# Optimization experiments

Measured on AMD Instinct MI355X. Metric: run time of the kernel, lower is better.

## Reference

```python
import jax, jax.numpy as jnp
import numpy as np
from jax import lax

R, K = 1000, 80                 # proposals per image, foreground classes
IMG_H, IMG_W = 800.0, 1333.0    # image_shape (h, w) used by Boxes.clip
SCORE_THRESH = 0.05
NMS_THRESH = 0.5
TOPK = 100                      # topk_per_image


def setup_inputs() -> dict:
    key = jax.random.key(0)
    k1, k2, k3 = jax.random.split(key, 3)
    # well-formed class-specific boxes: x1y1 + positive wh
    x1y1 = jax.random.uniform(k1, (R, K, 2)) * jnp.array([IMG_W - 60.0, IMG_H - 60.0])
    wh = jax.random.uniform(k2, (R, K, 2)) * 200.0 + 10.0
    boxes = jnp.concatenate([x1y1, x1y1 + wh], axis=-1).reshape(R, K * 4)
    logits = jax.random.normal(k3, (R, K + 1)) * 2.0
    scores = jax.nn.softmax(logits, axis=-1)  # (R, K+1), last col = background
    return {"boxes": boxes, "scores": scores}


def _iou_matrix(b):
    # b: [R, 4] (x1, y1, x2, y2) -> [R, R] pairwise IoU
    x1, y1, x2, y2 = b[:, 0], b[:, 1], b[:, 2], b[:, 3]
    area = jnp.clip(x2 - x1, 0.0) * jnp.clip(y2 - y1, 0.0)
    xx1 = jnp.maximum(x1[:, None], x1[None, :])
    yy1 = jnp.maximum(y1[:, None], y1[None, :])
    xx2 = jnp.minimum(x2[:, None], x2[None, :])
    yy2 = jnp.minimum(y2[:, None], y2[None, :])
    inter = jnp.clip(xx2 - xx1, 0.0) * jnp.clip(yy2 - yy1, 0.0)
    union = area[:, None] + area[None, :] - inter
    return inter / jnp.maximum(union, 1e-9)


def _nms_one_class(boxes_c, scores_c, valid_c):
    # boxes_c: [R,4], scores_c: [R], valid_c: [R] bool (passed score filter)
    masked = jnp.where(valid_c, scores_c, -jnp.inf)
    order = jnp.argsort(-masked)            # descending score
    b = boxes_c[order]
    s = masked[order]
    v = valid_c[order]
    iou = iou_full = _iou_matrix(b)          # [R, R]
    idx = jnp.arange(R)

    def body(i, keep):
        # box i (if still kept & valid) suppresses later boxes with high IoU
        sup = (iou_full[i] > NMS_THRESH) & keep[i] & (idx > i)
        return keep & ~sup

    keep = lax.fori_loop(0, R, body, v)
    return s, keep, order


def reference(boxes, scores):
    # boxes: (R, K*4), scores: (R, K+1)
    bx = boxes.reshape(R, K, 4)
    # Boxes.clip(image_shape=(h, w)): x in [0, w], y in [0, h]
    bx = jnp.stack([
        jnp.clip(bx[..., 0], 0.0, IMG_W),
        jnp.clip(bx[..., 1], 0.0, IMG_H),
        jnp.clip(bx[..., 2], 0.0, IMG_W),
        jnp.clip(bx[..., 3], 0.0, IMG_H),
    ], axis=-1)

    fg = scores[:, :-1]                                  # (R, K) foreground scores
    thres = jnp.minimum(SCORE_THRESH, (fg.mean() + fg.max()) / 2.0)
    valid = fg > thres                                   # filter_mask

    # per-class batched NMS (equivalent to torchvision batched_nms)
    boxes_k = jnp.transpose(bx, (1, 0, 2))               # [K, R, 4]
    s_sorted, keep, order = jax.vmap(_nms_one_class)(boxes_k, fg.T, valid.T)

    flat = jnp.where(keep, s_sorted, -jnp.inf).reshape(-1)   # [K*R]
    topv, topi = lax.top_k(flat, TOPK)                   # keep[:topk], score-sorted
    cls = topi // R
    pos = topi % R
    prop = order[cls, pos]                               # original proposal index (filter_inds[:,0])
    ok = jnp.isfinite(topv)
    okf = ok.astype(boxes.dtype)

    box_out = bx[prop, cls] * okf[:, None]               # pred_boxes  [TOPK, 4]
    sc_out = jnp.where(ok, topv, 0.0)                    # scores      [TOPK]
    full_out = scores[prop] * okf[:, None]               # full_scores [TOPK, K+1]
    cls_out = (cls * ok).astype(boxes.dtype)             # pred_classes as float col

    # packed result: [boxes(4) | score(1) | class(1) | full_scores(K+1)]
    return jnp.concatenate([box_out, sc_out[:, None], cls_out[:, None], full_out], axis=1)
```

## Files before the change

### kernel.cpp

```cpp
#include <hip/hip_runtime.h>
#include <stdint.h>

typedef unsigned long long u64;
typedef unsigned int u32;

#define R_N 1000
#define K_N 80
#define NCOL 81
#define TOPK_N 100
#define OUT_W 87
#define IMG_W_ 1333.0f
#define IMG_H_ 800.0f
#define CSTR 100
#define CSTRP 101
#define NQUAD ((R_N * NCOL) / 4)
#define NMAX 448
#define WMAX 7
#define KM (K_N * CSTR)
#define POISON 0xAAAAAAAAu

__device__ __forceinline__ u32 f32_order(float f) {
    u32 u = __float_as_uint(f);
    return u ^ (((u32)((int)u >> 31)) | 0x80000000u);
}
__device__ __forceinline__ float f32_unorder(u32 o) {
    u32 u = (o & 0x80000000u) ? (o ^ 0x80000000u) : ~o;
    return __uint_as_float(u);
}

__device__ __forceinline__ void grid_barrier(u32* bar, u32 nblk) {
    __syncthreads();
    if (threadIdx.x == 0) {
        __threadfence();
        if (__hip_atomic_load(bar, __ATOMIC_RELAXED, __HIP_MEMORY_SCOPE_AGENT) == POISON)
            atomicCAS(bar, POISON, 0u);
        __hip_atomic_fetch_add(bar, 1u, __ATOMIC_ACQ_REL, __HIP_MEMORY_SCOPE_AGENT);
        while (__hip_atomic_load(bar, __ATOMIC_ACQUIRE, __HIP_MEMORY_SCOPE_AGENT) < nblk)
            __builtin_amdgcn_s_sleep(2);
    }
    __syncthreads();
}

struct P2 {
    float4 bx4[R_N];
    u64 key_s[R_N];
    u64 pool[NMAX * WMAX];
    float area[R_N];
    u64 keep_words[16];
    int s_n;
};
struct P3 {
    u64 keys[K_N * CSTRP];
    int rnk[TOPK_N];
    u64 wx[TOPK_N];
    int wr[TOPK_N];
    int wn;
};
union SMEM { P2 p2; P3 p3; };

__device__ void run_nms_cold(int c, int tid, int lane, int wv, u64 below, float th,
                             const float* __restrict__ scores, P2& p2,
                             const float* __restrict__ boxes, u64* __restrict__ cand,
                             u32* __restrict__ kbs) {
    u64* ukey = p2.pool;
    if (wv == 0) {
        float sval[16];
#pragma unroll
        for (int e = 0; e < 16; ++e) {
            int r = e * 64 + lane;
            sval[e] = (r < R_N) ? scores[r * NCOL + c] : -1e30f;
        }
        int nn = 0;
#pragma unroll
        for (int e = 0; e < 16; ++e) {
            bool pred = sval[e] > th;
            u64 m = __ballot(pred);
            if (pred) {
                int r = e * 64 + lane;
                ukey[nn + __popcll(m & below)] =
                    ((u64)f32_order(sval[e]) << 32) | (u64)(u32)(R_N - 1 - r);
            }
            nn += __popcll(m);
        }
        if (lane == 0) p2.s_n = nn;
    }
    __syncthreads();
    const int n = p2.s_n;

    for (int j = tid; j < n; j += 256) {
        u64 kj = ukey[j];
        int rank = 0;
        for (int k = 0; k < n; ++k) rank += (ukey[k] > kj) ? 1 : 0;
        int r = (R_N - 1) - (int)(kj & 0xFFFFFFFFull);
        float4 b = ((const float4*)boxes)[r * K_N + c];
        float x1 = fminf(fmaxf(b.x, 0.f), IMG_W_);
        float y1 = fminf(fmaxf(b.y, 0.f), IMG_H_);
        float x2 = fminf(fmaxf(b.z, 0.f), IMG_W_);
        float y2 = fminf(fmaxf(b.w, 0.f), IMG_H_);
        p2.key_s[rank] = kj;
        p2.bx4[rank] = make_float4(x1, y1, x2, y2);
        p2.area[rank] = fmaxf(x2 - x1, 0.f) * fmaxf(y2 - y1, 0.f);
    }
    __syncthreads();

    if (n <= NMAX) {
        const int W = (n + 63) >> 6;
        u64* Mrow = p2.pool;
        const int nh = n >> 1;
        for (int t2 = wv; t2 < 2 * W; t2 += 4) {
            int w = t2 >> 1, ih = t2 & 1;
            int i0 = ih ? nh : 0;
            int i1 = ih ? n : nh;
            int j = w * 64 + lane;
            bool jv = j < n;
            float4 bj = jv ? p2.bx4[j] : make_float4(0.f, 0.f, 0.f, 0.f);
            float aj = jv ? p2.area[j] : 0.f;
            for (int i = i0; i < i1; ++i) {
                float4 bi = p2.bx4[i];
                float ai = p2.area[i];
                float xx1 = fmaxf(bi.x, bj.x), yy1 = fmaxf(bi.y, bj.y);
                float xx2 = fminf(bi.z, bj.z), yy2 = fminf(bi.w, bj.w);
                float inter = fmaxf(xx2 - xx1, 0.f) * fmaxf(yy2 - yy1, 0.f);
                bool sup = jv && (j > i) &&
                           (inter / fmaxf(ai + aj - inter, 1e-9f) > 0.5f);
                u64 m = __ballot(sup);
                if (lane == 0) Mrow[i * W + w] = m;
            }
        }
        __syncthreads();

        if (wv == 0) {
            u64 keep_w = 0;
            if (lane < W) {
                int rem = n - lane * 64;
                keep_w = (rem >= 64) ? ~0ull : ((1ull << rem) - 1ull);
            }
            const int lw = (lane < W) ? lane : 0;
            u64 fifo[8];
#pragma unroll
            for (int d = 0; d < 8; ++d) fifo[d] = (d < n) ? Mrow[d * W + lw] : 0ull;
            for (int ib = 0; ib < n; ib += 8) {
#pragma unroll
                for (int d = 0; d < 8; ++d) {
                    int i = ib + d;
                    if (i >= n) break;
                    u64 row = fifo[d];
                    int ip = i + 8;
                    fifo[d] = (ip < n) ? Mrow[ip * W + lw] : 0ull;
                    u64 kw = __shfl(keep_w, i >> 6);
                    if ((kw >> (i & 63)) & 1ull) keep_w &= ~row;
                }
            }
            if (lane < W) p2.keep_words[lane] = keep_w;
            if (lane >= W && lane < 16) p2.keep_words[lane] = 0;
        }
    } else {
        int* keep = (int*)p2.pool;
        for (int j = tid; j < n; j += 256) keep[j] = 1;
        __syncthreads();
        for (int i = 0; i < n - 1; ++i) {
            __syncthreads();
            if (!keep[i]) continue;
            float4 bi = p2.bx4[i];
            float ai = p2.area[i];
            for (int j = i + 1 + tid; j < n; j += 256) {
                if (!keep[j]) continue;
                float xx1 = fmaxf(bi.x, p2.bx4[j].x), yy1 = fmaxf(bi.y, p2.bx4[j].y);
                float xx2 = fminf(bi.z, p2.bx4[j].z), yy2 = fminf(bi.w, p2.bx4[j].w);
                float inter = fmaxf(xx2 - xx1, 0.f) * fmaxf(yy2 - yy1, 0.f);
                if (inter / fmaxf(ai + p2.area[j] - inter, 1e-9f) > 0.5f) keep[j] = 0;
            }
        }
        __syncthreads();
        if (wv == 0) {
            for (int w = 0; w < 16; ++w) {
                int j = w * 64 + lane;
                u64 m = __ballot((j < n) && keep[j]);
                if (lane == 0) p2.keep_words[w] = m;
            }
        }
    }
    __syncthreads();

    if (wv == 0) {
        int kb = 0;
        for (int j0 = 0; j0 < n; j0 += 64) {
            int j = j0 + lane;
            u64 mw = p2.keep_words[j0 >> 6];
            bool kp = (j < n) && ((mw >> lane) & 1ull);
            u64 mm = __ballot(kp);
            int kr = kb + __popcll(mm & below);
            if (kp && kr < CSTR) {
                u64 kj = p2.key_s[j];
                u32 osc = (u32)(kj >> 32);
                int rr = (R_N - 1) - (int)(kj & 0xFFFFFFFFull);
                int flat = c * R_N + j;
                cand[c * CSTR + kr] =
                    ((u64)osc << 27) | ((u64)(u32)(131071 - flat) << 10) | (u64)(u32)rr;
            }
            kb += __popcll(mm);
        }
        if (kb > CSTR) kb = CSTR;
        if (lane == 0) kbs[c] = (u32)kb;
        for (int kz = kb + lane; kz < CSTR; kz += 64) cand[c * CSTR + kz] = 0;
    }
}

__global__ __launch_bounds__(256, 1) void k_nms(const float* __restrict__ boxes,
                                                const float* __restrict__ scores,
                                                float* __restrict__ hdr,
                                                u32* __restrict__ kbs,
                                                u64* __restrict__ cand) {
    __shared__ P2 p2;
    __shared__ float s_sum[4], s_max[4];

    const int bid = blockIdx.x, tid = threadIdx.x;
    const int lane = tid & 63, wv = tid >> 6;
    const int c = bid;
    const u64 below = (lane == 0) ? 0ull : (~0ull >> (64 - lane));

    float sval[16];
    if (wv == 0) {
#pragma unroll
        for (int e = 0; e < 16; ++e) {
            int r = e * 64 + lane;
            sval[e] = (r < R_N) ? scores[r * NCOL + c] : -1e30f;
        }
    }
    float4 breg[4];
#pragma unroll
    for (int e = 0; e < 4; ++e) {
        int r = tid + e * 256;
        breg[e] = (r < R_N) ? ((const float4*)boxes)[r * K_N + c]
                            : make_float4(0.f, 0.f, 0.f, 0.f);
    }
    const int q = bid * 256 + tid;
    float4 qv = (q < NQUAD) ? ((const float4*)scores)[q]
                            : make_float4(0.f, 0.f, 0.f, 0.f);

    {
        float sum = 0.f, mx = -1e30f;
        if (q < NQUAD) {
            int m = (q * 4) % NCOL;
            float vv[4] = {qv.x, qv.y, qv.z, qv.w};
#pragma unroll
            for (int e = 0; e < 4; ++e) {
                int mm = m + e; if (mm >= NCOL) mm -= NCOL;
                if (mm != K_N) { sum += vv[e]; mx = fmaxf(mx, vv[e]); }
            }
        }
#pragma unroll
        for (int off = 32; off > 0; off >>= 1) {
            sum += __shfl_down(sum, off);
            mx = fmaxf(mx, __shfl_down(mx, off));
        }
        if (lane == 0) { s_sum[wv] = sum; s_max[wv] = mx; }
    }

    float4* bstage = (float4*)p2.pool;
#pragma unroll
    for (int e = 0; e < 4; ++e) {
        int r = tid + e * 256;
        if (r < R_N) bstage[r] = breg[e];
    }
    u64* ukey = p2.pool + 2000;
    if (wv == 0) {
        int nn = 0;
#pragma unroll
        for (int e = 0; e < 16; ++e) {
            bool pred = sval[e] > 0.05f;
            u64 m = __ballot(pred);
            if (pred) {
                int r = e * 64 + lane;
                ukey[nn + __popcll(m & below)] =
                    ((u64)f32_order(sval[e]) << 32) | (u64)(u32)(R_N - 1 - r);
            }
            nn += __popcll(m);
        }
        if (lane == 0) p2.s_n = nn;
    }
    __syncthreads();
    if (tid == 0) {
        hdr[2 * bid] = s_sum[0] + s_sum[1] + s_sum[2] + s_sum[3];
        hdr[2 * bid + 1] = fmaxf(fmaxf(s_max[0], s_max[1]), fmaxf(s_max[2], s_max[3]));
    }
    const int n = p2.s_n;

    for (int j = tid; j < n; j += 256) {
        u64 kj = ukey[j];
        int rank = 0;
        for (int k = 0; k < n; ++k) rank += (ukey[k] > kj) ? 1 : 0;
        int r = (R_N - 1) - (int)(kj & 0xFFFFFFFFull);
        float4 b = bstage[r];
        float x1 = fminf(fmaxf(b.x, 0.f), IMG_W_);
        float y1 = fminf(fmaxf(b.y, 0.f), IMG_H_);
        float x2 = fminf(fmaxf(b.z, 0.f), IMG_W_);
        float y2 = fminf(fmaxf(b.w, 0.f), IMG_H_);
        p2.key_s[rank] = kj;
        p2.bx4[rank] = make_float4(x1, y1, x2, y2);
        p2.area[rank] = fmaxf(x2 - x1, 0.f) * fmaxf(y2 - y1, 0.f);
    }
    __syncthreads();

    if (n <= NMAX) {
        const int W = (n + 63) >> 6;
        u64* Mrow = p2.pool;
        for (int t2 = wv; t2 < 4 * W; t2 += 4) {
            int w = t2 >> 2, qh = t2 & 3;
            int i0 = (n * qh) >> 2;
            int i1 = (n * (qh + 1)) >> 2;
            int j = w * 64 + lane;
            bool jv = j < n;
            float4 bj = jv ? p2.bx4[j] : make_float4(0.f, 0.f, 0.f, 0.f);
            float aj = jv ? p2.area[j] : 0.f;
            for (int i = i0; i < i1; ++i) {
                float4 bi = p2.bx4[i];
                float ai = p2.area[i];
                float xx1 = fmaxf(bi.x, bj.x), yy1 = fmaxf(bi.y, bj.y);
                float xx2 = fminf(bi.z, bj.z), yy2 = fminf(bi.w, bj.w);
                float inter = fmaxf(xx2 - xx1, 0.f) * fmaxf(yy2 - yy1, 0.f);
                bool sup = jv && (j > i) &&
                           (inter / fmaxf(ai + aj - inter, 1e-9f) > 0.5f);
                u64 m = __ballot(sup);
                if (lane == 0) Mrow[i * W + w] = m;
            }
        }
        __syncthreads();

        if (wv == 0) {
            u64 keep_w = 0;
            if (lane < W) {
                int rem = n - lane * 64;
                keep_w = (rem >= 64) ? ~0ull : ((1ull << rem) - 1ull);
            }
            const int lw = (lane < W) ? lane : 0;
            u64 fifo[8];
#pragma unroll
            for (int d = 0; d < 8; ++d) fifo[d] = (d < n) ? Mrow[d * W + lw] : 0ull;
            for (int ib = 0; ib < n; ib += 8) {
#pragma unroll
                for (int d = 0; d < 8; ++d) {
                    int i = ib + d;
                    if (i >= n) break;
                    u64 row = fifo[d];
                    int ip = i + 8;
                    fifo[d] = (ip < n) ? Mrow[ip * W + lw] : 0ull;
                    u64 kw = __shfl(keep_w, i >> 6);
                    if ((kw >> (i & 63)) & 1ull) keep_w &= ~row;
                }
            }
            if (lane < W) p2.keep_words[lane] = keep_w;
            if (lane >= W && lane < 16) p2.keep_words[lane] = 0;
        }
    } else {
        int* keep = (int*)p2.pool;
        for (int j = tid; j < n; j += 256) keep[j] = 1;
        __syncthreads();
        for (int i = 0; i < n - 1; ++i) {
            __syncthreads();
            if (!keep[i]) continue;
            float4 bi = p2.bx4[i];
            float ai = p2.area[i];
            for (int j = i + 1 + tid; j < n; j += 256) {
                if (!keep[j]) continue;
                float xx1 = fmaxf(bi.x, p2.bx4[j].x), yy1 = fmaxf(bi.y, p2.bx4[j].y);
                float xx2 = fminf(bi.z, p2.bx4[j].z), yy2 = fminf(bi.w, p2.bx4[j].w);
                float inter = fmaxf(xx2 - xx1, 0.f) * fmaxf(yy2 - yy1, 0.f);
                if (inter / fmaxf(ai + p2.area[j] - inter, 1e-9f) > 0.5f) keep[j] = 0;
            }
        }
        __syncthreads();
        if (wv == 0) {
            for (int w = 0; w < 16; ++w) {
                int j = w * 64 + lane;
                u64 m = __ballot((j < n) && keep[j]);
                if (lane == 0) p2.keep_words[w] = m;
            }
        }
    }

    if (wv == 0) {
        int kb = 0;
        for (int j0 = 0; j0 < n; j0 += 64) {
            int j = j0 + lane;
            u64 mw = p2.keep_words[j0 >> 6];
            bool kp = (j < n) && ((mw >> lane) & 1ull);
            u64 mm = __ballot(kp);
            int kr = kb + __popcll(mm & below);
            if (kp && kr < CSTR) {
                u64 kj = p2.key_s[j];
                u32 osc = (u32)(kj >> 32);
                int rr = (R_N - 1) - (int)(kj & 0xFFFFFFFFull);
                int flat = c * R_N + j;
                cand[c * CSTR + kr] =
                    ((u64)osc << 27) | ((u64)(u32)(131071 - flat) << 10) | (u64)(u32)rr;
            }
            kb += __popcll(mm);
        }
        if (kb > CSTR) kb = CSTR;
        if (lane == 0) kbs[c] = (u32)kb;
        for (int kz = kb + lane; kz < CSTR; kz += 64) cand[c * CSTR + kz] = 0;
    }
}

__global__ __launch_bounds__(256, 1) void k_top(const float* __restrict__ boxes,
                                                const float* __restrict__ scores,
                                                float* __restrict__ hdr,
                                                u32* __restrict__ kbs,
                                                u32* __restrict__ bars,
                                                u64* __restrict__ cand,
                                                float* __restrict__ outp) {
    __shared__ SMEM sm;
    __shared__ int s_cnt[2];
    __shared__ int s_kbc;
    __shared__ float s_thres;

    const int bid = blockIdx.x, tid = threadIdx.x;
    const int lane = tid & 63, wv = tid >> 6;
    const int c = bid;
    const u64 below = (lane == 0) ? 0ull : (~0ull >> (64 - lane));

    {
        const ulonglong2* cp = (const ulonglong2*)cand;
        for (int t = tid; t < KM / 2; t += 256) {
            ulonglong2 v = cp[t];
            int e0 = 2 * t;
            int cc2 = e0 / CSTR, pos = e0 - cc2 * CSTR;
            sm.p3.keys[cc2 * CSTRP + pos] = v.x;
            sm.p3.keys[cc2 * CSTRP + pos + 1] = v.y;
        }
    }
    u32 kcnt = (tid < K_N) ? kbs[tid] : 0u;
    if (tid == c) s_kbc = (int)kcnt;
    {
        int cnt = (int)kcnt;
#pragma unroll
        for (int off = 32; off > 0; off >>= 1) cnt += __shfl_down(cnt, off);
        if (lane == 0 && wv < 2) s_cnt[wv] = cnt;
    }
    if (wv == 0) {
        float S = hdr[2 * lane], M = hdr[2 * lane + 1];
        if (lane + 64 < K_N) {
            S += hdr[2 * (lane + 64)];
            M = fmaxf(M, hdr[2 * (lane + 64) + 1]);
        }
#pragma unroll
        for (int off = 32; off > 0; off >>= 1) {
            S += __shfl_down(S, off);
            M = fmaxf(M, __shfl_down(M, off));
        }
        if (lane == 0)
            s_thres = fminf(0.05f, 0.5f * (S / (float)(R_N * K_N) + M));
    }
    __syncthreads();
    int total = s_cnt[0] + s_cnt[1];

    if (s_thres != 0.05f) {
        const float th = s_thres;
        run_nms_cold(c, tid, lane, wv, below, th, scores, sm.p2, boxes, cand, kbs);
        grid_barrier(&bars[0], K_N);
        {
            const ulonglong2* cp = (const ulonglong2*)cand;
            for (int t = tid; t < KM / 2; t += 256) {
                ulonglong2 v = cp[t];
                int e0 = 2 * t;
                int cc2 = e0 / CSTR, pos = e0 - cc2 * CSTR;
                sm.p3.keys[cc2 * CSTRP + pos] = v.x;
                sm.p3.keys[cc2 * CSTRP + pos + 1] = v.y;
            }
            int cnt = (tid < K_N) ? (int)kbs[tid] : 0;
            if (tid == c) s_kbc = cnt;
#pragma unroll
            for (int off = 32; off > 0; off >>= 1) cnt += __shfl_down(cnt, off);
            if (lane == 0 && wv < 2) s_cnt[wv] = cnt;
        }
        __syncthreads();
        total = s_cnt[0] + s_cnt[1];
    }

    const int target = total < TOPK_N ? total : TOPK_N;
    const int kb = s_kbc;

    if (tid < TOPK_N) sm.p3.rnk[tid] = tid;
    if (tid == 0) sm.p3.wn = 0;
    __syncthreads();

    const int TASKS = kb * (K_N - 1);
    for (int g = 0; g * 2048 < TASKS; ++g) {
        int lo[8], hi[8], ii[8], base[8];
        u64 xv[8];
        bool act[8];
#pragma unroll
        for (int s = 0; s < 8; ++s) {
            int t = g * 2048 + s * 256 + tid;
            act[s] = t < TASKS;
            int i = 0, cc2 = 0;
            if (act[s]) { i = t % kb; cc2 = t / kb; }
            cc2 += (cc2 >= c);
            ii[s] = i;
            base[s] = cc2 * CSTRP;
            xv[s] = sm.p3.keys[c * CSTRP + i];
            if (xv[s] == 0ull) act[s] = false;
            lo[s] = 0; hi[s] = CSTR;
        }
#pragma unroll
        for (int st = 0; st < 7; ++st) {
#pragma unroll
            for (int s = 0; s < 8; ++s) {
                int mid = (lo[s] + hi[s]) >> 1;
                u64 v = sm.p3.keys[base[s] + mid];
                bool live = lo[s] < hi[s];
                bool gt = live && (v > xv[s]);
                lo[s] = gt ? mid + 1 : lo[s];
                hi[s] = (live && !gt) ? mid : hi[s];
            }
        }
#pragma unroll
        for (int s = 0; s < 8; ++s)
            if (act[s] && lo[s] > 0) atomicAdd(&sm.p3.rnk[ii[s]], lo[s]);
    }
    __syncthreads();

    if (tid < kb) {
        int r = sm.p3.rnk[tid];
        if (r < target) {
            int idx = atomicAdd(&sm.p3.wn, 1);
            sm.p3.wx[idx] = sm.p3.keys[c * CSTRP + tid];
            sm.p3.wr[idx] = r;
        }
    }
    __syncthreads();
    const int wn = sm.p3.wn;

    for (int e = tid; e < wn * OUT_W; e += 256) {
        int w = e / OUT_W, col = e - w * OUT_W;
        u64 x = sm.p3.wx[w];
        int r = sm.p3.wr[w];
        int prop = (int)(x & 0x3FFull);
        float val;
        if (col < 4) {
            float b = boxes[prop * (K_N * 4) + c * 4 + col];
            float lim = (col & 1) ? IMG_H_ : IMG_W_;
            val = fminf(fmaxf(b, 0.f), lim);
        } else if (col == 4) {
            val = f32_unorder((u32)((x >> 27) & 0xFFFFFFFFull));
        } else if (col == 5) {
            val = (float)c;
        } else {
            val = scores[prop * NCOL + (col - 6)];
        }
        outp[r * OUT_W + col] = val;
    }
    for (int row = target + bid; row < TOPK_N; row += K_N) {
        int ob = row * OUT_W;
        for (int e = tid; e < OUT_W; e += 256) outp[ob + e] = 0.f;
    }
}

extern "C" void kernel_launch(void* const* d_in, const int* in_sizes, int n_in,
                              void* d_out, int out_size, void* d_ws, size_t ws_size,
                              hipStream_t stream) {
    const float* boxes = (const float*)d_in[0];
    const float* scores = (const float*)d_in[1];
    float* hdr = (float*)d_ws;
    u32* kbs = (u32*)((char*)d_ws + 640);
    u32* bars = (u32*)((char*)d_ws + 960);
    u64* cand = (u64*)((char*)d_ws + 1024);

    k_nms<<<dim3(K_N), dim3(256), 0, stream>>>(boxes, scores, hdr, kbs, cand);
    k_top<<<dim3(K_N), dim3(256), 0, stream>>>(boxes, scores, hdr, kbs, bars, cand, (float*)d_out);
}
```

Measured before the change: 93.98 us.

## Fuse NMS and top-k kernels into one launch with flag-based cross-block sync

Merges the per-class NMS kernel and the top-k/output kernel into a single launch. Inter-block dependencies (threshold stats, per-class keep counts) are now handled by per-entry poison-sentinel flags that consumers spin on, replacing the second launch and the grid barrier. The threshold reduction runs on a second wavefront while wave 0 does suppression. This saves one launch and its gap. It relies on all 80 blocks being co-resident and on the workspace being reset to the poison value before each call.

```diff
diff --git a/kernel.cpp b/kernel.cpp
--- a/kernel.cpp
+++ b/kernel.cpp
@@ -28,41 +28,72 @@
     return __uint_as_float(u);
 }
 
-__device__ __forceinline__ void grid_barrier(u32* bar, u32 nblk) {
-    __syncthreads();
-    if (threadIdx.x == 0) {
-        __threadfence();
-        if (__hip_atomic_load(bar, __ATOMIC_RELAXED, __HIP_MEMORY_SCOPE_AGENT) == POISON)
-            atomicCAS(bar, POISON, 0u);
-        __hip_atomic_fetch_add(bar, 1u, __ATOMIC_ACQ_REL, __HIP_MEMORY_SCOPE_AGENT);
-        while (__hip_atomic_load(bar, __ATOMIC_ACQUIRE, __HIP_MEMORY_SCOPE_AGENT) < nblk)
-            __builtin_amdgcn_s_sleep(2);
-    }
-    __syncthreads();
-}
-
-struct P2 {
-    float4 bx4[R_N];
-    u64 key_s[R_N];
-    u64 pool[NMAX * WMAX];
-    float area[R_N];
-    u64 keep_words[16];
-    int s_n;
-};
-struct P3 {
-    u64 keys[K_N * CSTRP];
-    int rnk[TOPK_N];
-    u64 wx[TOPK_N];
-    int wr[TOPK_N];
-    int wn;
-};
-union SMEM { P2 p2; P3 p3; };
+__device__ __forceinline__ void emit_keep(int c, int lane, u64 below, int n,
+                                          const u64* key_s, const u64* keep_words,
+                                          u64* __restrict__ cand,
+                                          u32* __restrict__ flag, int* s_kbc_p) {
+    int kb = 0;
+    for (int j0 = 0; j0 < n; j0 += 64) {
+        int j = j0 + lane;
+        u64 mw = keep_words[j0 >> 6];
+        bool kp = (j < n) && ((mw >> lane) & 1ull);
+        u64 mm = __ballot(kp);
+        int kr = kb + __popcll(mm & below);
+        if (kp && kr < CSTR) {
+            u64 kj = key_s[j];
+            u32 osc = (u32)(kj >> 32);
+            int rr = (R_N - 1) - (int)(kj & 0xFFFFFFFFull);
+            int flat = c * R_N + j;
+            cand[c * CSTR + kr] =
+                ((u64)osc << 27) | ((u64)(u32)(131071 - flat) << 10) | (u64)(u32)rr;
+        }
+        kb += __popcll(mm);
+    }
+    if (kb > CSTR) kb = CSTR;
+    if (lane == 0) *s_kbc_p = kb;
+    for (int kz = kb + lane; kz < CSTR; kz += 64) cand[c * CSTR + kz] = 0;
+    __threadfence();
+    if (lane == 0)
+        __hip_atomic_store(&flag[c], (u32)kb, __ATOMIC_RELAXED, __HIP_MEMORY_SCOPE_AGENT);
+}
+
+__device__ __forceinline__ void calc_thres(int lane, const u32* __restrict__ hdru,
+                                           float* s_thres_p) {
+    u32 u0, u1;
+    for (;;) { u0 = __hip_atomic_load(&hdru[2 * lane], __ATOMIC_ACQUIRE,
+                                      __HIP_MEMORY_SCOPE_AGENT);
+               if (u0 != POISON) break; __builtin_amdgcn_s_sleep(1); }
+    for (;;) { u1 = __hip_atomic_load(&hdru[2 * lane + 1], __ATOMIC_ACQUIRE,
+                                      __HIP_MEMORY_SCOPE_AGENT);
+               if (u1 != POISON) break; __builtin_amdgcn_s_sleep(1); }
+    float S = __uint_as_float(u0), M = __uint_as_float(u1);
+    if (lane < K_N - 64) {
+        u32 v0, v1;
+        for (;;) { v0 = __hip_atomic_load(&hdru[2 * (lane + 64)], __ATOMIC_ACQUIRE,
+                                          __HIP_MEMORY_SCOPE_AGENT);
+                   if (v0 != POISON) break; __builtin_amdgcn_s_sleep(1); }
+        for (;;) { v1 = __hip_atomic_load(&hdru[2 * (lane + 64) + 1], __ATOMIC_ACQUIRE,
+                                          __HIP_MEMORY_SCOPE_AGENT);
+                   if (v1 != POISON) break; __builtin_amdgcn_s_sleep(1); }
+        S += __uint_as_float(v0);
+        M = fmaxf(M, __uint_as_float(v1));
+    }
+#pragma unroll
+    for (int off = 32; off > 0; off >>= 1) {
+        S += __shfl_down(S, off);
+        M = fmaxf(M, __shfl_down(M, off));
+    }
+    if (lane == 0)
+        *s_thres_p = fminf(0.05f, 0.5f * (S / (float)(R_N * K_N) + M));
+}
 
 __device__ void run_nms_cold(int c, int tid, int lane, int wv, u64 below, float th,
-                             const float* __restrict__ scores, P2& p2,
-                             const float* __restrict__ boxes, u64* __restrict__ cand,
-                             u32* __restrict__ kbs) {
-    u64* ukey = p2.pool;
+                             const float* __restrict__ scores,
+                             const float* __restrict__ boxes,
+                             u64* __restrict__ cand, u32* __restrict__ flag,
+                             float4* bx4, u64* key_s, u64* pool, float* area,
+                             u64* keep_words, int* s_n_p, int* s_kbc_p) {
+    u64* ukey = pool;
     if (wv == 0) {
         float sval[16];
 #pragma unroll
@@ -82,10 +113,10 @@
             }
             nn += __popcll(m);
         }
-        if (lane == 0) p2.s_n = nn;
-    }
-    __syncthreads();
-    const int n = p2.s_n;
+        if (lane == 0) *s_n_p = nn;
+    }
+    __syncthreads();
+    const int n = *s_n_p;
 
     for (int j = tid; j < n; j += 256) {
         u64 kj = ukey[j];
@@ -97,27 +128,26 @@
         float y1 = fminf(fmaxf(b.y, 0.f), IMG_H_);
         float x2 = fminf(fmaxf(b.z, 0.f), IMG_W_);
         float y2 = fminf(fmaxf(b.w, 0.f), IMG_H_);
-        p2.key_s[rank] = kj;
-        p2.bx4[rank] = make_float4(x1, y1, x2, y2);
-        p2.area[rank] = fmaxf(x2 - x1, 0.f) * fmaxf(y2 - y1, 0.f);
+        key_s[rank] = kj;
+        bx4[rank] = make_float4(x1, y1, x2, y2);
+        area[rank] = fmaxf(x2 - x1, 0.f) * fmaxf(y2 - y1, 0.f);
     }
     __syncthreads();
 
     if (n <= NMAX) {
         const int W = (n + 63) >> 6;
-        u64* Mrow = p2.pool;
-        const int nh = n >> 1;
-        for (int t2 = wv; t2 < 2 * W; t2 += 4) {
-            int w = t2 >> 1, ih = t2 & 1;
-            int i0 = ih ? nh : 0;
-            int i1 = ih ? n : nh;
+        u64* Mrow = pool;
+        for (int t2 = wv; t2 < 4 * W; t2 += 4) {
+            int w = t2 >> 2, qh = t2 & 3;
+            int i0 = (n * qh) >> 2;
+            int i1 = (n * (qh + 1)) >> 2;
             int j = w * 64 + lane;
             bool jv = j < n;
-            float4 bj = jv ? p2.bx4[j] : make_float4(0.f, 0.f, 0.f, 0.f);
-            float aj = jv ? p2.area[j] : 0.f;
+            float4 bj = jv ? bx4[j] : make_float4(0.f, 0.f, 0.f, 0.f);
+            float aj = jv ? area[j] : 0.f;
             for (int i = i0; i < i1; ++i) {
-                float4 bi = p2.bx4[i];
-                float ai = p2.area[i];
+                float4 bi = bx4[i];
+                float ai = area[i];
                 float xx1 = fmaxf(bi.x, bj.x), yy1 = fmaxf(bi.y, bj.y);
                 float xx2 = fminf(bi.z, bj.z), yy2 = fminf(bi.w, bj.w);
                 float inter = fmaxf(xx2 - xx1, 0.f) * fmaxf(yy2 - yy1, 0.f);
@@ -151,24 +181,25 @@
                     if ((kw >> (i & 63)) & 1ull) keep_w &= ~row;
                 }
             }
-            if (lane < W) p2.keep_words[lane] = keep_w;
-            if (lane >= W && lane < 16) p2.keep_words[lane] = 0;
+            if (lane < W) keep_words[lane] = keep_w;
+            if (lane >= W && lane < 16) keep_words[lane] = 0;
+            emit_keep(c, lane, below, n, key_s, keep_words, cand, flag, s_kbc_p);
         }
     } else {
-        int* keep = (int*)p2.pool;
+        int* keep = (int*)pool;
         for (int j = tid; j < n; j += 256) keep[j] = 1;
         __syncthreads();
         for (int i = 0; i < n - 1; ++i) {
             __syncthreads();
             if (!keep[i]) continue;
-            float4 bi = p2.bx4[i];
-            float ai = p2.area[i];
+            float4 bi = bx4[i];
+            float ai = area[i];
             for (int j = i + 1 + tid; j < n; j += 256) {
                 if (!keep[j]) continue;
-                float xx1 = fmaxf(bi.x, p2.bx4[j].x), yy1 = fmaxf(bi.y, p2.bx4[j].y);
-                float xx2 = fminf(bi.z, p2.bx4[j].z), yy2 = fminf(bi.w, p2.bx4[j].w);
+                float xx1 = fmaxf(bi.x, bx4[j].x), yy1 = fmaxf(bi.y, bx4[j].y);
+                float xx2 = fminf(bi.z, bx4[j].z), yy2 = fminf(bi.w, bx4[j].w);
                 float inter = fmaxf(xx2 - xx1, 0.f) * fmaxf(yy2 - yy1, 0.f);
-                if (inter / fmaxf(ai + p2.area[j] - inter, 1e-9f) > 0.5f) keep[j] = 0;
+                if (inter / fmaxf(ai + area[j] - inter, 1e-9f) > 0.5f) keep[j] = 0;
             }
         }
         __syncthreads();
@@ -176,43 +207,33 @@
             for (int w = 0; w < 16; ++w) {
                 int j = w * 64 + lane;
                 u64 m = __ballot((j < n) && keep[j]);
-                if (lane == 0) p2.keep_words[w] = m;
-            }
-        }
-    }
-    __syncthreads();
-
-    if (wv == 0) {
-        int kb = 0;
-        for (int j0 = 0; j0 < n; j0 += 64) {
-            int j = j0 + lane;
-            u64 mw = p2.keep_words[j0 >> 6];
-            bool kp = (j < n) && ((mw >> lane) & 1ull);
-            u64 mm = __ballot(kp);
-            int kr = kb + __popcll(mm & below);
-            if (kp && kr < CSTR) {
-                u64 kj = p2.key_s[j];
-                u32 osc = (u32)(kj >> 32);
-                int rr = (R_N - 1) - (int)(kj & 0xFFFFFFFFull);
-                int flat = c * R_N + j;
-                cand[c * CSTR + kr] =
-                    ((u64)osc << 27) | ((u64)(u32)(131071 - flat) << 10) | (u64)(u32)rr;
-            }
-            kb += __popcll(mm);
-        }
-        if (kb > CSTR) kb = CSTR;
-        if (lane == 0) kbs[c] = (u32)kb;
-        for (int kz = kb + lane; kz < CSTR; kz += 64) cand[c * CSTR + kz] = 0;
-    }
-}
-
-__global__ __launch_bounds__(256, 1) void k_nms(const float* __restrict__ boxes,
+                if (lane == 0) keep_words[w] = m;
+            }
+            emit_keep(c, lane, below, n, key_s, keep_words, cand, flag, s_kbc_p);
+        }
+    }
+}
+
+__global__ __launch_bounds__(256, 1) void k_all(const float* __restrict__ boxes,
                                                 const float* __restrict__ scores,
-                                                float* __restrict__ hdr,
-                                                u32* __restrict__ kbs,
-                                                u64* __restrict__ cand) {
-    __shared__ P2 p2;
-    __shared__ float s_sum[4], s_max[4];
+                                                u32* __restrict__ hdru,
+                                                u32* __restrict__ kbs0,
+                                                u32* __restrict__ kbs1,
+                                                u64* __restrict__ cand,
+                                                float* __restrict__ outp) {
+    __shared__ union {
+        struct { float4 bx4[R_N]; float area[R_N]; u64 pool[NMAX * WMAX]; } a;
+        u64 keys[K_N * CSTRP];
+    } u;
+    __shared__ u64 key_s[R_N];
+    __shared__ u64 keep_words[16];
+    __shared__ int s_n;
+    __shared__ float s_sum[4], s_max[4], s_thres;
+    __shared__ int s_cnt[2], s_kbc;
+    __shared__ int rnk[TOPK_N];
+    __shared__ u64 wx[TOPK_N];
+    __shared__ int wr[TOPK_N];
+    __shared__ int wn;
 
     const int bid = blockIdx.x, tid = threadIdx.x;
     const int lane = tid & 63, wv = tid >> 6;
@@ -257,13 +278,13 @@
         if (lane == 0) { s_sum[wv] = sum; s_max[wv] = mx; }
     }
 
-    float4* bstage = (float4*)p2.pool;
+    float4* bstage = (float4*)u.a.pool;
 #pragma unroll
     for (int e = 0; e < 4; ++e) {
         int r = tid + e * 256;
         if (r < R_N) bstage[r] = breg[e];
     }
-    u64* ukey = p2.pool + 2000;
+    u64* ukey = u.a.pool + 2000;
     if (wv == 0) {
         int nn = 0;
 #pragma unroll
@@ -277,14 +298,18 @@
             }
             nn += __popcll(m);
         }
-        if (lane == 0) p2.s_n = nn;
+        if (lane == 0) s_n = nn;
     }
     __syncthreads();
     if (tid == 0) {
-        hdr[2 * bid] = s_sum[0] + s_sum[1] + s_sum[2] + s_sum[3];
-        hdr[2 * bid + 1] = fmaxf(fmaxf(s_max[0], s_max[1]), fmaxf(s_max[2], s_max[3]));
-    }
-    const int n = p2.s_n;
+        float S4 = s_sum[0] + s_sum[1] + s_sum[2] + s_sum[3];
+        float M4 = fmaxf(fmaxf(s_max[0], s_max[1]), fmaxf(s_max[2], s_max[3]));
+        __hip_atomic_store(&hdru[2 * c], __float_as_uint(S4),
+                           __ATOMIC_RELAXED, __HIP_MEMORY_SCOPE_AGENT);
+        __hip_atomic_store(&hdru[2 * c + 1], __float_as_uint(M4),
+                           __ATOMIC_RELAXED, __HIP_MEMORY_SCOPE_AGENT);
+    }
+    const int n = s_n;
 
     for (int j = tid; j < n; j += 256) {
         u64 kj = ukey[j];
@@ -296,26 +321,26 @@
         float y1 = fminf(fmaxf(b.y, 0.f), IMG_H_);
         float x2 = fminf(fmaxf(b.z, 0.f), IMG_W_);
         float y2 = fminf(fmaxf(b.w, 0.f), IMG_H_);
-        p2.key_s[rank] = kj;
-        p2.bx4[rank] = make_float4(x1, y1, x2, y2);
-        p2.area[rank] = fmaxf(x2 - x1, 0.f) * fmaxf(y2 - y1, 0.f);
+        key_s[rank] = kj;
+        u.a.bx4[rank] = make_float4(x1, y1, x2, y2);
+        u.a.area[rank] = fmaxf(x2 - x1, 0.f) * fmaxf(y2 - y1, 0.f);
     }
     __syncthreads();
 
     if (n <= NMAX) {
         const int W = (n + 63) >> 6;
-        u64* Mrow = p2.pool;
+        u64* Mrow = u.a.pool;
         for (int t2 = wv; t2 < 4 * W; t2 += 4) {
             int w = t2 >> 2, qh = t2 & 3;
             int i0 = (n * qh) >> 2;
             int i1 = (n * (qh + 1)) >> 2;
             int j = w * 64 + lane;
             bool jv = j < n;
-            float4 bj = jv ? p2.bx4[j] : make_float4(0.f, 0.f, 0.f, 0.f);
-            float aj = jv ? p2.area[j] : 0.f;
+            float4 bj = jv ? u.a.bx4[j] : make_float4(0.f, 0.f, 0.f, 0.f);
+            float aj = jv ? u.a.area[j] : 0.f;
             for (int i = i0; i < i1; ++i) {
-                float4 bi = p2.bx4[i];
-                float ai = p2.area[i];
+                float4 bi = u.a.bx4[i];
+                float ai = u.a.area[i];
                 float xx1 = fmaxf(bi.x, bj.x), yy1 = fmaxf(bi.y, bj.y);
                 float xx2 = fminf(bi.z, bj.z), yy2 = fminf(bi.w, bj.w);
                 float inter = fmaxf(xx2 - xx1, 0.f) * fmaxf(yy2 - yy1, 0.f);
@@ -349,24 +374,27 @@
                     if ((kw >> (i & 63)) & 1ull) keep_w &= ~row;
                 }
             }
-            if (lane < W) p2.keep_words[lane] = keep_w;
-            if (lane >= W && lane < 16) p2.keep_words[lane] = 0;
+            if (lane < W) keep_words[lane] = keep_w;
+            if (lane >= W && lane < 16) keep_words[lane] = 0;
+            emit_keep(c, lane, below, n, key_s, keep_words, cand, kbs0, &s_kbc);
+        } else if (wv == 1) {
+            calc_thres(lane, hdru, &s_thres);
         }
     } else {
-        int* keep = (int*)p2.pool;
+        int* keep = (int*)u.a.pool;
         for (int j = tid; j < n; j += 256) keep[j] = 1;
         __syncthreads();
         for (int i = 0; i < n - 1; ++i) {
             __syncthreads();
             if (!keep[i]) continue;
-            float4 bi = p2.bx4[i];
-            float ai = p2.area[i];
+            float4 bi = u.a.bx4[i];
+            float ai = u.a.area[i];
             for (int j = i + 1 + tid; j < n; j += 256) {
                 if (!keep[j]) continue;
-                float xx1 = fmaxf(bi.x, p2.bx4[j].x), yy1 = fmaxf(bi.y, p2.bx4[j].y);
-                float xx2 = fminf(bi.z, p2.bx4[j].z), yy2 = fminf(bi.w, p2.bx4[j].w);
+                float xx1 = fmaxf(bi.x, u.a.bx4[j].x), yy1 = fmaxf(bi.y, u.a.bx4[j].y);
+                float xx2 = fminf(bi.z, u.a.bx4[j].z), yy2 = fminf(bi.w, u.a.bx4[j].w);
                 float inter = fmaxf(xx2 - xx1, 0.f) * fmaxf(yy2 - yy1, 0.f);
-                if (inter / fmaxf(ai + p2.area[j] - inter, 1e-9f) > 0.5f) keep[j] = 0;
+                if (inter / fmaxf(ai + u.a.area[j] - inter, 1e-9f) > 0.5f) keep[j] = 0;
             }
         }
         __syncthreads();
@@ -374,51 +402,46 @@
             for (int w = 0; w < 16; ++w) {
                 int j = w * 64 + lane;
                 u64 m = __ballot((j < n) && keep[j]);
-                if (lane == 0) p2.keep_words[w] = m;
-            }
-        }
-    }
-
-    if (wv == 0) {
-        int kb = 0;
-        for (int j0 = 0; j0 < n; j0 += 64) {
-            int j = j0 + lane;
-            u64 mw = p2.keep_words[j0 >> 6];
-            bool kp = (j < n) && ((mw >> lane) & 1ull);
-            u64 mm = __ballot(kp);
-            int kr = kb + __popcll(mm & below);
-            if (kp && kr < CSTR) {
-                u64 kj = p2.key_s[j];
-                u32 osc = (u32)(kj >> 32);
-                int rr = (R_N - 1) - (int)(kj & 0xFFFFFFFFull);
-                int flat = c * R_N + j;
-                cand[c * CSTR + kr] =
-                    ((u64)osc << 27) | ((u64)(u32)(131071 - flat) << 10) | (u64)(u32)rr;
-            }
-            kb += __popcll(mm);
-        }
-        if (kb > CSTR) kb = CSTR;
-        if (lane == 0) kbs[c] = (u32)kb;
-        for (int kz = kb + lane; kz < CSTR; kz += 64) cand[c * CSTR + kz] = 0;
-    }
-}
-
-__global__ __launch_bounds__(256, 1) void k_top(const float* __restrict__ boxes,
-                                                const float* __restrict__ scores,
-                                                float* __restrict__ hdr,
-                                                u32* __restrict__ kbs,
-                                                u32* __restrict__ bars,
-                                                u64* __restrict__ cand,
-                                                float* __restrict__ outp) {
-    __shared__ SMEM sm;
-    __shared__ int s_cnt[2];
-    __shared__ int s_kbc;
-    __shared__ float s_thres;
-
-    const int bid = blockIdx.x, tid = threadIdx.x;
-    const int lane = tid & 63, wv = tid >> 6;
-    const int c = bid;
-    const u64 below = (lane == 0) ? 0ull : (~0ull >> (64 - lane));
+                if (lane == 0) keep_words[w] = m;
+            }
+            emit_keep(c, lane, below, n, key_s, keep_words, cand, kbs0, &s_kbc);
+        } else if (wv == 1) {
+            calc_thres(lane, hdru, &s_thres);
+        }
+    }
+    __syncthreads();
+
+    u32 kcnt = 0;
+    const float th = s_thres;
+    if (th != 0.05f) {
+        run_nms_cold(c, tid, lane, wv, below, th, scores, boxes, cand, kbs1,
+                     u.a.bx4, key_s, u.a.pool, u.a.area, keep_words, &s_n, &s_kbc);
+        if (tid < K_N) {
+            for (;;) {
+                kcnt = __hip_atomic_load(&kbs1[tid], __ATOMIC_ACQUIRE,
+                                         __HIP_MEMORY_SCOPE_AGENT);
+                if (kcnt != POISON) break;
+                __builtin_amdgcn_s_sleep(1);
+            }
+        }
+    } else {
+        if (tid < K_N) {
+            for (;;) {
+                kcnt = __hip_atomic_load(&kbs0[tid], __ATOMIC_ACQUIRE,
+                                         __HIP_MEMORY_SCOPE_AGENT);
+                if (kcnt != POISON) break;
+                __builtin_amdgcn_s_sleep(1);
+            }
+        }
+    }
+    {
+        int cnt = (tid < K_N) ? (int)kcnt : 0;
+#pragma unroll
+        for (int off = 32; off > 0; off >>= 1) cnt += __shfl_down(cnt, off);
+        if (lane == 0 && wv < 2) s_cnt[wv] = cnt;
+    }
+    __syncthreads();
+    __threadfence();
 
     {
         const ulonglong2* cp = (const ulonglong2*)cand;
@@ -426,64 +449,17 @@
             ulonglong2 v = cp[t];
             int e0 = 2 * t;
             int cc2 = e0 / CSTR, pos = e0 - cc2 * CSTR;
-            sm.p3.keys[cc2 * CSTRP + pos] = v.x;
-            sm.p3.keys[cc2 * CSTRP + pos + 1] = v.y;
-        }
-    }
-    u32 kcnt = (tid < K_N) ? kbs[tid] : 0u;
-    if (tid == c) s_kbc = (int)kcnt;
-    {
-        int cnt = (int)kcnt;
-#pragma unroll
-        for (int off = 32; off > 0; off >>= 1) cnt += __shfl_down(cnt, off);
-        if (lane == 0 && wv < 2) s_cnt[wv] = cnt;
-    }
-    if (wv == 0) {
-        float S = hdr[2 * lane], M = hdr[2 * lane + 1];
-        if (lane + 64 < K_N) {
-            S += hdr[2 * (lane + 64)];
-            M = fmaxf(M, hdr[2 * (lane + 64) + 1]);
-        }
-#pragma unroll
-        for (int off = 32; off > 0; off >>= 1) {
-            S += __shfl_down(S, off);
-            M = fmaxf(M, __shfl_down(M, off));
-        }
-        if (lane == 0)
-            s_thres = fminf(0.05f, 0.5f * (S / (float)(R_N * K_N) + M));
-    }
-    __syncthreads();
-    int total = s_cnt[0] + s_cnt[1];
-
-    if (s_thres != 0.05f) {
-        const float th = s_thres;
-        run_nms_cold(c, tid, lane, wv, below, th, scores, sm.p2, boxes, cand, kbs);
-        grid_barrier(&bars[0], K_N);
-        {
-            const ulonglong2* cp = (const ulonglong2*)cand;
-            for (int t = tid; t < KM / 2; t += 256) {
-                ulonglong2 v = cp[t];
-                int e0 = 2 * t;
-                int cc2 = e0 / CSTR, pos = e0 - cc2 * CSTR;
-                sm.p3.keys[cc2 * CSTRP + pos] = v.x;
-                sm.p3.keys[cc2 * CSTRP + pos + 1] = v.y;
-            }
-            int cnt = (tid < K_N) ? (int)kbs[tid] : 0;
-            if (tid == c) s_kbc = cnt;
-#pragma unroll
-            for (int off = 32; off > 0; off >>= 1) cnt += __shfl_down(cnt, off);
-            if (lane == 0 && wv < 2) s_cnt[wv] = cnt;
-        }
-        __syncthreads();
-        total = s_cnt[0] + s_cnt[1];
-    }
-
+            u.keys[cc2 * CSTRP + pos] = v.x;
+            u.keys[cc2 * CSTRP + pos + 1] = v.y;
+        }
+    }
+    if (tid < TOPK_N) rnk[tid] = tid;
+    if (tid == 0) wn = 0;
+    __syncthreads();
+
+    const int total = s_cnt[0] + s_cnt[1];
     const int target = total < TOPK_N ? total : TOPK_N;
     const int kb = s_kbc;
-
-    if (tid < TOPK_N) sm.p3.rnk[tid] = tid;
-    if (tid == 0) sm.p3.wn = 0;
-    __syncthreads();
 
     const int TASKS = kb * (K_N - 1);
     for (int g = 0; g * 2048 < TASKS; ++g) {
@@ -499,7 +475,7 @@
             cc2 += (cc2 >= c);
             ii[s] = i;
             base[s] = cc2 * CSTRP;
-            xv[s] = sm.p3.keys[c * CSTRP + i];
+            xv[s] = u.keys[c * CSTRP + i];
             if (xv[s] == 0ull) act[s] = false;
             lo[s] = 0; hi[s] = CSTR;
         }
@@ -508,7 +484,7 @@
 #pragma unroll
             for (int s = 0; s < 8; ++s) {
                 int mid = (lo[s] + hi[s]) >> 1;
-                u64 v = sm.p3.keys[base[s] + mid];
+                u64 v = u.keys[base[s] + mid];
                 bool live = lo[s] < hi[s];
                 bool gt = live && (v > xv[s]);
                 lo[s] = gt ? mid + 1 : lo[s];
@@ -517,25 +493,25 @@
         }
 #pragma unroll
         for (int s = 0; s < 8; ++s)
-            if (act[s] && lo[s] > 0) atomicAdd(&sm.p3.rnk[ii[s]], lo[s]);
+            if (act[s] && lo[s] > 0) atomicAdd(&rnk[ii[s]], lo[s]);
     }
     __syncthreads();
 
     if (tid < kb) {
-        int r = sm.p3.rnk[tid];
+        int r = rnk[tid];
         if (r < target) {
-            int idx = atomicAdd(&sm.p3.wn, 1);
-            sm.p3.wx[idx] = sm.p3.keys[c * CSTRP + tid];
-            sm.p3.wr[idx] = r;
-        }
-    }
-    __syncthreads();
-    const int wn = sm.p3.wn;
-
-    for (int e = tid; e < wn * OUT_W; e += 256) {
+            int idx = atomicAdd(&wn, 1);
+            wx[idx] = u.keys[c * CSTRP + tid];
+            wr[idx] = r;
+        }
+    }
+    __syncthreads();
+    const int wnl = wn;
+
+    for (int e = tid; e < wnl * OUT_W; e += 256) {
         int w = e / OUT_W, col = e - w * OUT_W;
-        u64 x = sm.p3.wx[w];
-        int r = sm.p3.wr[w];
+        u64 x = wx[w];
+        int r = wr[w];
         int prop = (int)(x & 0x3FFull);
         float val;
         if (col < 4) {
@@ -562,11 +538,11 @@
                               hipStream_t stream) {
     const float* boxes = (const float*)d_in[0];
     const float* scores = (const float*)d_in[1];
-    float* hdr = (float*)d_ws;
-    u32* kbs = (u32*)((char*)d_ws + 640);
-    u32* bars = (u32*)((char*)d_ws + 960);
-    u64* cand = (u64*)((char*)d_ws + 1024);
-
-    k_nms<<<dim3(K_N), dim3(256), 0, stream>>>(boxes, scores, hdr, kbs, cand);
-    k_top<<<dim3(K_N), dim3(256), 0, stream>>>(boxes, scores, hdr, kbs, bars, cand, (float*)d_out);
-}
+    u32* hdru = (u32*)d_ws;
+    u32* kbs0 = (u32*)((char*)d_ws + 640);
+    u32* kbs1 = (u32*)((char*)d_ws + 960);
+    u64* cand = (u64*)((char*)d_ws + 1280);
+
+    k_all<<<dim3(K_N), dim3(256), 0, stream>>>(boxes, scores, hdru, kbs0, kbs1,
+                                               cand, (float*)d_out);
+}
```

After: 99.74 us. +6.1%, slower.
